# Kernel optimization log

Hardware: AMD Instinct MI355X
Metric: run time of the kernel (lower is better)

Reference implementation:

```python
import jax, jax.numpy as jnp
import numpy as np

SQRT_2_OVER_PI = 0.7978845608028654

def gelu_tanh(x):
    return 0.5 * x * (1.0 + jnp.tanh(SQRT_2_OVER_PI * (x + 0.044715 * x ** 3)))

def setup_inputs() -> dict:
    key = jax.random.key(0)
    ks = jax.random.split(key, 16)
    B, L, H, Dk, Dv = 4, 512, 8, 64, 64
    dm = H * Dk
    inp = {
        'q': jax.random.normal(ks[0], (B, L, dm), jnp.float32),
        'k': jax.random.normal(ks[1], (B, L, dm), jnp.float32),
        'v': jax.random.normal(ks[2], (B, L, dm), jnp.float32),
        'vec_adj_k': jax.random.normal(ks[3], (B, L, L, Dk), jnp.float32),
        'vec_adj_v': jax.random.normal(ks[4], (B, L, L, Dv), jnp.float32),
        'adj_k': jax.random.randint(ks[5], (B, L, L), 0, 2, jnp.int32),
        'adj_v': jax.random.randint(ks[6], (B, L, L), 0, 2, jnp.int32),
        # learned params (Linear weights stored as [in, out]; y = x @ W)
        'w_qs': jax.random.normal(ks[7], (dm, H * Dk), jnp.float32) * 0.02,
        'w_ks': jax.random.normal(ks[8], (dm, H * Dk), jnp.float32) * 0.02,
        'w_vs': jax.random.normal(ks[9], (dm, H * Dv), jnp.float32) * 0.02,
        'w_fc': jax.random.normal(ks[10], (H * Dk, H * Dk), jnp.float32) * 0.02,
        'w_nw': jax.random.normal(ks[11], (H * Dk, 1), jnp.float32) * 0.02,
        'w_self': jax.random.normal(ks[12], (H * Dk, H * Dk), jnp.float32) * 0.02,
        'w_dd': jax.random.normal(ks[13], (H * Dk, H * Dk), jnp.float32) * 0.02,
    }
    return inp

def reference(q, k, v, vec_adj_k, vec_adj_v, adj_k, adj_v,
              w_qs, w_ks, w_vs, w_fc, w_nw, w_self, w_dd):
    H, Dk, Dv = 8, 64, 64
    B, L, dm = q.shape
    temperature = Dk ** 0.5
    residual = q
    # projections -> [B, H, L, D]
    qh = (q @ w_qs).reshape(B, L, H, Dk).transpose(0, 2, 1, 3)
    kh = (k @ w_ks).reshape(B, L, H, Dk).transpose(0, 2, 1, 3)
    vh = (v @ w_vs).reshape(B, L, H, Dv).transpose(0, 2, 1, 3)
    qs = qh / temperature
    # inner_(q, k, vec_adj_k, flag=True): content + relative-position scores
    scores = jnp.einsum('bhld,bhmd->bhlm', qs, kh) \
           + jnp.einsum('bhld,blmd->bhlm', qs, vec_adj_k)  # [B,H,L,L]
    # adjacency mask (mask == 0 -> -10000)
    scores = jnp.where(adj_k[:, None, :, :] == 0, jnp.float32(-10000.0), scores)
    attn = jax.nn.softmax(scores, axis=-1)
    # inner_(attn, v, vec_adj_v, flag=False)
    out = jnp.einsum('bhlm,bhmd->bhld', attn, vh) \
        + jnp.einsum('bhlm,blmd->bhld', attn, vec_adj_v)
    qc = out.transpose(0, 2, 1, 3).reshape(B, L, H * Dv)  # [B,L,dm]
    # masked neighbor aggregation (GNN stage)
    adj_f = adj_k.astype(qc.dtype)
    nn_num = adj_f.sum(-1)                                  # [B,L]
    denom = jnp.where(nn_num >= 1.0, nn_num, 1.0)
    node_weight = jax.nn.sigmoid((qc @ w_nw)[..., 0])       # [B,L]
    self_info = qc @ w_self
    dd_info = qc @ w_dd
    dd_weight = node_weight[:, None, :] * adj_f             # [B,L,L]
    agg = jnp.matmul(dd_weight, dd_info) / denom[..., None]
    qo = gelu_tanh((self_info + agg) @ w_fc)
    qo = residual + qo
    return (qo, attn)
```

## Files before the change

kernel.cpp:

```cpp
#include <hip/hip_runtime.h>
#include <cstdint>

#define NB 4
#define NL 512
#define NH 8
#define ND 64
#define NDM 512

typedef __attribute__((ext_vector_type(8))) short short8;
typedef __attribute__((ext_vector_type(4))) float f32x4;

__device__ __forceinline__ unsigned short f2bf(float f){
  union { float f; unsigned u; } v; v.f = f;
  unsigned r = (v.u + 0x7fffu + ((v.u >> 16) & 1u)) >> 16;
  return (unsigned short)r;
}

__device__ __forceinline__ short8 ld8(const unsigned short* p){
  return *(const short8*)p;
}

__device__ __forceinline__ f32x4 mfma16(short8 a, short8 b, f32x4 c){
  return __builtin_amdgcn_mfma_f32_16x16x32_bf16(a, b, c, 0, 0, 0);
}

__device__ __forceinline__ float gelu_tanh(float x){
  float u = 0.7978845608028654f * (x + 0.044715f * x * x * x);
  return 0.5f * x * (1.f + tanhf(u));
}

__global__ __launch_bounds__(256) void k_cvt_in(const float* __restrict__ q,
    const float* __restrict__ k, const float* __restrict__ v,
    unsigned short* __restrict__ dst){
  int i = blockIdx.x * 256 + threadIdx.x;
  int w = i >> 18, r = i & 262143;
  const float* src = (w == 0) ? q : (w == 1) ? k : v;
  float4 f = *(const float4*)(src + (size_t)r * 4);
  unsigned lo = (unsigned)f2bf(f.x) | ((unsigned)f2bf(f.y) << 16);
  unsigned hi = (unsigned)f2bf(f.z) | ((unsigned)f2bf(f.w) << 16);
  uint2 o; o.x = lo; o.y = hi;
  *(uint2*)(dst + (size_t)w * 1048576 + (size_t)r * 4) = o;
}

__global__ __launch_bounds__(256) void k_cvt_w(const float* __restrict__ wqs,
    const float* __restrict__ wks, const float* __restrict__ wvs,
    const float* __restrict__ wself, const float* __restrict__ wdd,
    const float* __restrict__ wfc, unsigned short* __restrict__ Wt){
  int i = blockIdx.x * 256 + threadIdx.x;
  int w = i >> 18, r = i & 262143;
  const float* src = (w == 0) ? wqs : (w == 1) ? wks : (w == 2) ? wvs :
                     (w == 3) ? wself : (w == 4) ? wdd : wfc;
  int kk = r >> 9, n = r & 511;
  Wt[(size_t)w * 262144 + (size_t)n * 512 + kk] = f2bf(src[r]);
}

__global__ __launch_bounds__(256) void k_proj(const unsigned short* __restrict__ X,
    const unsigned short* __restrict__ W, unsigned short* __restrict__ dst, int mode){
  int wid = blockIdx.x * 4 + (threadIdx.x >> 6);
  int lane = threadIdx.x & 63;
  int tm = wid >> 5, tn = wid & 31;
  int r = lane & 15, q = lane >> 4;
  const unsigned short* A  = X + (size_t)(tm * 16 + r) * 512 + q * 8;
  const unsigned short* Bp = W + (size_t)(tn * 16 + r) * 512 + q * 8;
  f32x4 acc = {0.f, 0.f, 0.f, 0.f};
  for (int k = 0; k < 512; k += 32) acc = mfma16(ld8(A + k), ld8(Bp + k), acc);
  int col = tn * 16 + r;
  int h = col >> 6, d = col & 63;
  float sc = (mode == 0) ? 0.125f : 1.0f;
  for (int i = 0; i < 4; i++){
    int row = tm * 16 + q * 4 + i;
    int b = row >> 9, l = row & 511;
    float vv = acc[i] * sc;
    size_t idx = (mode == 2) ? ((size_t)((b * 8 + h) * 64 + d) * 512 + l)
                             : ((size_t)((b * 8 + h) * 512 + l) * 64 + d);
    dst[idx] = f2bf(vv);
  }
}

__global__ __launch_bounds__(256) void k_scores(const unsigned short* __restrict__ qs,
    const unsigned short* __restrict__ kh, float* __restrict__ attnF){
  int wid = blockIdx.x * 4 + (threadIdx.x >> 6);
  int lane = threadIdx.x & 63;
  int bh = wid >> 10, tile = wid & 1023;
  int tm = tile >> 5, tn = tile & 31;
  int r = lane & 15, q = lane >> 4;
  const unsigned short* A  = qs + (size_t)bh * 512 * 64 + (size_t)(tm * 16 + r) * 64 + q * 8;
  const unsigned short* Bp = kh + (size_t)bh * 512 * 64 + (size_t)(tn * 16 + r) * 64 + q * 8;
  f32x4 acc = {0.f, 0.f, 0.f, 0.f};
  acc = mfma16(ld8(A),      ld8(Bp),      acc);
  acc = mfma16(ld8(A + 32), ld8(Bp + 32), acc);
  float* C = attnF + (size_t)bh * 512 * 512;
  for (int i = 0; i < 4; i++){
    int row = tm * 16 + q * 4 + i;
    C[(size_t)row * 512 + tn * 16 + r] = acc[i];
  }
}

__global__ __launch_bounds__(256) void k_relsoft(const unsigned short* __restrict__ qs,
    const float* __restrict__ vak, const int* __restrict__ adj,
    float* __restrict__ attnF, unsigned short* __restrict__ attn_bf){
  int bid = blockIdx.x;
  int b = bid >> 9, l = bid & 511;
  int t = threadIdx.x, lane = t & 63, w = t >> 6;
  __shared__ __align__(16) unsigned short qsA[16 * 64];
  __shared__ __align__(16) unsigned short vkt[128 * 72];
  __shared__ float sc[8 * 512];
  __shared__ int adjs[512];
  for (int j = 0; j < 4; j++){
    int e = t + j * 256;
    int m = e >> 6, d = e & 63;
    qsA[e] = (m < 8) ? qs[((size_t)((b * 8 + m) * 512 + l)) * 64 + d] : (unsigned short)0;
  }
  for (int j = 0; j < 16; j++){
    int e = t + j * 256;
    int h = e >> 9, m = e & 511;
    sc[e] = attnF[((size_t)(b * 8 + h) * 512 + l) * 512 + m];
  }
  adjs[t]       = adj[(size_t)bid * 512 + t];
  adjs[t + 256] = adj[(size_t)bid * 512 + t + 256];
  __syncthreads();
  int r = lane & 15, q = lane >> 4;
  short8 a0 = ld8(qsA + r * 64 + q * 8);
  short8 a1 = ld8(qsA + r * 64 + 32 + q * 8);
  const float* vrow = vak + (size_t)bid * 512 * 64;
  for (int c = 0; c < 4; c++){
    for (int it = 0; it < 16; it++){
      int i2 = it * 256 + t;
      int m = i2 >> 5, d2 = (i2 & 31) * 2;
      const float2 f = *(const float2*)(vrow + (size_t)(c * 128 + m) * 64 + d2);
      unsigned pack = (unsigned)f2bf(f.x) | ((unsigned)f2bf(f.y) << 16);
      *(unsigned*)(&vkt[m * 72 + d2]) = pack;
    }
    __syncthreads();
    for (int nt2 = 0; nt2 < 2; nt2++){
      int nt = w * 2 + nt2;
      const unsigned short* bp = vkt + (nt * 16 + r) * 72 + q * 8;
      f32x4 acc = {0.f, 0.f, 0.f, 0.f};
      acc = mfma16(a0, ld8(bp),      acc);
      acc = mfma16(a1, ld8(bp + 32), acc);
      if (q < 2){
        for (int i = 0; i < 4; i++){
          int h = q * 4 + i;
          sc[h * 512 + c * 128 + nt * 16 + r] += acc[i];
        }
      }
    }
    __syncthreads();
  }
  for (int hh = 0; hh < 2; hh++){
    int h = w * 2 + hh;
    float v[8]; float mx = -3.0e38f;
    for (int i = 0; i < 8; i++){
      int m = lane + i * 64;
      float s = sc[h * 512 + m];
      if (adjs[m] == 0) s = -10000.0f;
      v[i] = s; mx = fmaxf(mx, s);
    }
    for (int off = 32; off; off >>= 1) mx = fmaxf(mx, __shfl_xor(mx, off, 64));
    float sum = 0.f;
    for (int i = 0; i < 8; i++){ v[i] = __expf(v[i] - mx); sum += v[i]; }
    for (int off = 32; off; off >>= 1) sum += __shfl_xor(sum, off, 64);
    float inv = 1.f / sum;
    size_t base = ((size_t)(b * 8 + h) * 512 + l) * 512;
    for (int i = 0; i < 8; i++){
      int m = lane + i * 64;
      float p2 = v[i] * inv;
      attnF[base + m] = p2;
      attn_bf[base + m] = f2bf(p2);
    }
  }
}

__global__ __launch_bounds__(256) void k_outc(const unsigned short* __restrict__ attn_bf,
    const unsigned short* __restrict__ vhT, float* __restrict__ qc){
  int wid = blockIdx.x * 4 + (threadIdx.x >> 6);
  int lane = threadIdx.x & 63;
  int bh = wid >> 7, tile = wid & 127;
  int tm = tile >> 2, tn = tile & 3;
  int r = lane & 15, q = lane >> 4;
  const unsigned short* A  = attn_bf + (size_t)bh * 512 * 512 + (size_t)(tm * 16 + r) * 512 + q * 8;
  const unsigned short* Bp = vhT + (size_t)bh * 64 * 512 + (size_t)(tn * 16 + r) * 512 + q * 8;
  f32x4 acc = {0.f, 0.f, 0.f, 0.f};
  for (int k = 0; k < 512; k += 32) acc = mfma16(ld8(A + k), ld8(Bp + k), acc);
  int b = bh >> 3, h = bh & 7;
  int d = tn * 16 + r;
  for (int i = 0; i < 4; i++){
    int lrow = tm * 16 + q * 4 + i;
    qc[(size_t)(b * 512 + lrow) * 512 + h * 64 + d] = acc[i];
  }
}

__global__ __launch_bounds__(256) void k_outrel(const unsigned short* __restrict__ attn_bf,
    const float* __restrict__ vav, const float* __restrict__ qc,
    const int* __restrict__ adj, const float* __restrict__ wnw,
    unsigned short* __restrict__ qc_bf, float* __restrict__ nw, float* __restrict__ invden){
  int bid = blockIdx.x;
  int b = bid >> 9, l = bid & 511;
  int t = threadIdx.x, lane = t & 63, w = t >> 6;
  __shared__ __align__(16) unsigned short vvT[64 * 136];
  __shared__ float orL[512];
  __shared__ float redf[4];
  __shared__ int redi[4];
  int r = lane & 15, q = lane >> 4;
  int h8 = r & 7;
  const float* vrow = vav + (size_t)bid * 512 * 64;
  const unsigned short* arow = attn_bf + ((size_t)(b * 8 + h8) * 512 + l) * 512;
  f32x4 acc = {0.f, 0.f, 0.f, 0.f};
  for (int c = 0; c < 4; c++){
    for (int it = 0; it < 16; it++){
      int i2 = it * 256 + t;
      int m = i2 >> 5, d2 = (i2 & 31) * 2;
      const float2 f = *(const float2*)(vrow + (size_t)(c * 128 + m) * 64 + d2);
      vvT[d2 * 136 + m]       = f2bf(f.x);
      vvT[(d2 + 1) * 136 + m] = f2bf(f.y);
    }
    __syncthreads();
    for (int s = 0; s < 4; s++){
      int kk = c * 128 + s * 32;
      short8 av = ld8(arow + kk + q * 8);
      short8 bv = ld8(vvT + (w * 16 + r) * 136 + s * 32 + q * 8);
      acc = mfma16(av, bv, acc);
    }
    __syncthreads();
  }
  if (q < 2){
    for (int i = 0; i < 4; i++){
      int h = q * 4 + i;
      orL[h * 64 + w * 16 + r] = acc[i];
    }
  }
  __syncthreads();
  float part = 0.f; int asum = 0;
  for (int j = 0; j < 2; j++){
    int e = t + j * 256;
    float val = qc[(size_t)bid * 512 + e] + orL[e];
    qc_bf[(size_t)bid * 512 + e] = f2bf(val);
    part += val * wnw[e];
    asum += adj[(size_t)bid * 512 + e];
  }
  for (int off = 32; off; off >>= 1){
    part += __shfl_xor(part, off, 64);
    asum += __shfl_xor(asum, off, 64);
  }
  if (lane == 0){ redf[w] = part; redi[w] = asum; }
  __syncthreads();
  if (t == 0){
    float tot = redf[0] + redf[1] + redf[2] + redf[3];
    int at = redi[0] + redi[1] + redi[2] + redi[3];
    nw[bid] = 1.f / (1.f + __expf(-tot));
    invden[bid] = 1.f / ((at >= 1) ? (float)at : 1.f);
  }
}

__global__ __launch_bounds__(256) void k_ddw(const int* __restrict__ adj,
    const float* __restrict__ nw, const float* __restrict__ invden,
    unsigned short* __restrict__ ddw){
  int i = blockIdx.x * 256 + threadIdx.x;
  int b = i >> 18, rest = i & 262143;
  int l = rest >> 9, m = rest & 511;
  int a = adj[i];
  float v = a ? nw[b * 512 + m] * invden[b * 512 + l] : 0.f;
  ddw[i] = f2bf(v);
}

__global__ __launch_bounds__(256) void k_gnn(const unsigned short* __restrict__ qcb,
    const unsigned short* __restrict__ W, float* __restrict__ outf,
    unsigned short* __restrict__ outT, int mode){
  int wid = blockIdx.x * 4 + (threadIdx.x >> 6);
  int lane = threadIdx.x & 63;
  int tm = wid >> 5, tn = wid & 31;
  int r = lane & 15, q = lane >> 4;
  const unsigned short* A  = qcb + (size_t)(tm * 16 + r) * 512 + q * 8;
  const unsigned short* Bp = W + (size_t)(tn * 16 + r) * 512 + q * 8;
  f32x4 acc = {0.f, 0.f, 0.f, 0.f};
  for (int k = 0; k < 512; k += 32) acc = mfma16(ld8(A + k), ld8(Bp + k), acc);
  int col = tn * 16 + r;
  for (int i = 0; i < 4; i++){
    int row = tm * 16 + q * 4 + i;
    if (mode == 0) outf[(size_t)row * 512 + col] = acc[i];
    else {
      int b = row >> 9, m = row & 511;
      outT[((size_t)(b * 512 + col)) * 512 + m] = f2bf(acc[i]);
    }
  }
}

__global__ __launch_bounds__(256) void k_agg(const unsigned short* __restrict__ ddw,
    const unsigned short* __restrict__ ddT, const float* __restrict__ selfi,
    unsigned short* __restrict__ xbf){
  int wid = blockIdx.x * 4 + (threadIdx.x >> 6);
  int lane = threadIdx.x & 63;
  int b = wid >> 10, tile = wid & 1023;
  int tm = tile >> 5, tn = tile & 31;
  int r = lane & 15, q = lane >> 4;
  const unsigned short* A  = ddw + (size_t)b * 262144 + (size_t)(tm * 16 + r) * 512 + q * 8;
  const unsigned short* Bp = ddT + (size_t)b * 262144 + (size_t)(tn * 16 + r) * 512 + q * 8;
  f32x4 acc = {0.f, 0.f, 0.f, 0.f};
  for (int k = 0; k < 512; k += 32) acc = mfma16(ld8(A + k), ld8(Bp + k), acc);
  int col = tn * 16 + r;
  for (int i = 0; i < 4; i++){
    int row = b * 512 + tm * 16 + q * 4 + i;
    float x = acc[i] + selfi[(size_t)row * 512 + col];
    xbf[(size_t)row * 512 + col] = f2bf(x);
  }
}

__global__ __launch_bounds__(256) void k_fc(const unsigned short* __restrict__ xbf,
    const unsigned short* __restrict__ W, const float* __restrict__ qin,
    float* __restrict__ qo){
  int wid = blockIdx.x * 4 + (threadIdx.x >> 6);
  int lane = threadIdx.x & 63;
  int tm = wid >> 5, tn = wid & 31;
  int r = lane & 15, q = lane >> 4;
  const unsigned short* A  = xbf + (size_t)(tm * 16 + r) * 512 + q * 8;
  const unsigned short* Bp = W + (size_t)(tn * 16 + r) * 512 + q * 8;
  f32x4 acc = {0.f, 0.f, 0.f, 0.f};
  for (int k = 0; k < 512; k += 32) acc = mfma16(ld8(A + k), ld8(Bp + k), acc);
  int col = tn * 16 + r;
  for (int i = 0; i < 4; i++){
    int row = tm * 16 + q * 4 + i;
    qo[(size_t)row * 512 + col] = qin[(size_t)row * 512 + col] + gelu_tanh(acc[i]);
  }
}

extern "C" void kernel_launch(void* const* d_in, const int* in_sizes, int n_in,
                              void* d_out, int out_size, void* d_ws, size_t ws_size,
                              hipStream_t stream){
  const float* q    = (const float*)d_in[0];
  const float* k    = (const float*)d_in[1];
  const float* v    = (const float*)d_in[2];
  const float* vak  = (const float*)d_in[3];
  const float* vav  = (const float*)d_in[4];
  const int*   adjk = (const int*)d_in[5];
  const float* wqs  = (const float*)d_in[7];
  const float* wks  = (const float*)d_in[8];
  const float* wvs  = (const float*)d_in[9];
  const float* wfc  = (const float*)d_in[10];
  const float* wnw  = (const float*)d_in[11];
  const float* wself= (const float*)d_in[12];
  const float* wdd  = (const float*)d_in[13];

  float* qo    = (float*)d_out;
  float* attnF = qo + 1048576;

  char* p = (char*)d_ws;
  unsigned short* xin   = (unsigned short*)p; p += 6291456;
  unsigned short* Wt    = (unsigned short*)p; p += 3145728;
  unsigned short* qsb   = (unsigned short*)p; p += 2097152;
  unsigned short* khb   = (unsigned short*)p; p += 2097152;
  unsigned short* vhT   = (unsigned short*)p; p += 2097152;
  unsigned short* attnb = (unsigned short*)p; p += 16777216;
  float*          qc    = (float*)p;          p += 4194304;
  unsigned short* qcb   = (unsigned short*)p; p += 2097152;
  float*          nw    = (float*)p;          p += 8192;
  float*          invd  = (float*)p;          p += 8192;
  float*          selfi = (float*)p;          p += 4194304;
  unsigned short* ddT   = (unsigned short*)p; p += 2097152;
  unsigned short* ddw   = (unsigned short*)p; p += 2097152;
  unsigned short* xbf   = (unsigned short*)p; p += 2097152;

  k_cvt_in<<<3072, 256, 0, stream>>>(q, k, v, xin);
  k_cvt_w<<<6144, 256, 0, stream>>>(wqs, wks, wvs, wself, wdd, wfc, Wt);
  k_proj<<<1024, 256, 0, stream>>>(xin,           Wt,          qsb, 0);
  k_proj<<<1024, 256, 0, stream>>>(xin + 1048576, Wt + 262144, khb, 1);
  k_proj<<<1024, 256, 0, stream>>>(xin + 2097152, Wt + 524288, vhT, 2);
  k_scores<<<8192, 256, 0, stream>>>(qsb, khb, attnF);
  k_relsoft<<<2048, 256, 0, stream>>>(qsb, vak, adjk, attnF, attnb);
  k_outc<<<1024, 256, 0, stream>>>(attnb, vhT, qc);
  k_outrel<<<2048, 256, 0, stream>>>(attnb, vav, qc, adjk, wnw, qcb, nw, invd);
  k_ddw<<<4096, 256, 0, stream>>>(adjk, nw, invd, ddw);
  k_gnn<<<1024, 256, 0, stream>>>(qcb, Wt + 786432,  selfi, (unsigned short*)nullptr, 0);
  k_gnn<<<1024, 256, 0, stream>>>(qcb, Wt + 1048576, (float*)nullptr, ddT, 1);
  k_agg<<<1024, 256, 0, stream>>>(ddw, ddT, selfi, xbf);
  k_fc<<<1024, 256, 0, stream>>>(xbf, Wt + 1310720, q, qo);
}
```

Before: 742.3 us.

## Fuse attention-value relative term into softmax kernel and merge launches

Moves the attn·vec_adj_v product into the softmax kernel, where the attention row is still in shared memory, so a separate pass no longer re-reads the bf16 attention. The vec_adj_k conversion now happens in registers and skips the LDS staging. Weight transposes go through a shared-memory tile for coalescing, and the input/weight conversions, the three projections and the two GNN GEMMs each become one launch. The ddw matrix is now built on the fly inside the aggregation GEMM. The new vec_adj_v loads are strided scalar reads, and the aggregation kernel recomputes the adjacency weights for every output column tile.

```diff
diff --git a/kernel.cpp b/kernel.cpp
--- a/kernel.cpp
+++ b/kernel.cpp
@@ -1,79 +1,87 @@
 #include <hip/hip_runtime.h>
 #include <cstdint>
 
-#define NB 4
-#define NL 512
-#define NH 8
-#define ND 64
-#define NDM 512
-
 typedef __attribute__((ext_vector_type(8))) short short8;
 typedef __attribute__((ext_vector_type(4))) float f32x4;
 
 __device__ __forceinline__ unsigned short f2bf(float f){
   union { float f; unsigned u; } v; v.f = f;
-  unsigned r = (v.u + 0x7fffu + ((v.u >> 16) & 1u)) >> 16;
-  return (unsigned short)r;
-}
-
-__device__ __forceinline__ short8 ld8(const unsigned short* p){
-  return *(const short8*)p;
-}
-
+  return (unsigned short)((v.u + 0x7fffu + ((v.u >> 16) & 1u)) >> 16);
+}
+__device__ __forceinline__ short8 ld8(const unsigned short* p){ return *(const short8*)p; }
 __device__ __forceinline__ f32x4 mfma16(short8 a, short8 b, f32x4 c){
   return __builtin_amdgcn_mfma_f32_16x16x32_bf16(a, b, c, 0, 0, 0);
 }
-
+__device__ __forceinline__ short8 cvt8(float4 a, float4 b){
+  short8 r;
+  r[0]=f2bf(a.x); r[1]=f2bf(a.y); r[2]=f2bf(a.z); r[3]=f2bf(a.w);
+  r[4]=f2bf(b.x); r[5]=f2bf(b.y); r[6]=f2bf(b.z); r[7]=f2bf(b.w);
+  return r;
+}
 __device__ __forceinline__ float gelu_tanh(float x){
   float u = 0.7978845608028654f * (x + 0.044715f * x * x * x);
   return 0.5f * x * (1.f + tanhf(u));
 }
 
-__global__ __launch_bounds__(256) void k_cvt_in(const float* __restrict__ q,
+__global__ __launch_bounds__(256) void k_prep(const float* __restrict__ q,
     const float* __restrict__ k, const float* __restrict__ v,
-    unsigned short* __restrict__ dst){
-  int i = blockIdx.x * 256 + threadIdx.x;
-  int w = i >> 18, r = i & 262143;
-  const float* src = (w == 0) ? q : (w == 1) ? k : v;
-  float4 f = *(const float4*)(src + (size_t)r * 4);
-  unsigned lo = (unsigned)f2bf(f.x) | ((unsigned)f2bf(f.y) << 16);
-  unsigned hi = (unsigned)f2bf(f.z) | ((unsigned)f2bf(f.w) << 16);
-  uint2 o; o.x = lo; o.y = hi;
-  *(uint2*)(dst + (size_t)w * 1048576 + (size_t)r * 4) = o;
-}
-
-__global__ __launch_bounds__(256) void k_cvt_w(const float* __restrict__ wqs,
-    const float* __restrict__ wks, const float* __restrict__ wvs,
-    const float* __restrict__ wself, const float* __restrict__ wdd,
-    const float* __restrict__ wfc, unsigned short* __restrict__ Wt){
-  int i = blockIdx.x * 256 + threadIdx.x;
-  int w = i >> 18, r = i & 262143;
-  const float* src = (w == 0) ? wqs : (w == 1) ? wks : (w == 2) ? wvs :
-                     (w == 3) ? wself : (w == 4) ? wdd : wfc;
-  int kk = r >> 9, n = r & 511;
-  Wt[(size_t)w * 262144 + (size_t)n * 512 + kk] = f2bf(src[r]);
-}
-
-__global__ __launch_bounds__(256) void k_proj(const unsigned short* __restrict__ X,
-    const unsigned short* __restrict__ W, unsigned short* __restrict__ dst, int mode){
-  int wid = blockIdx.x * 4 + (threadIdx.x >> 6);
+    const float* __restrict__ w0, const float* __restrict__ w1,
+    const float* __restrict__ w2, const float* __restrict__ w3,
+    const float* __restrict__ w4, const float* __restrict__ w5,
+    unsigned short* __restrict__ xin, unsigned short* __restrict__ Wt){
+  __shared__ unsigned short tl[64 * 72];
+  int bid = blockIdx.x, t = threadIdx.x;
+  if (bid < 3072){
+    int i = bid * 256 + t;
+    int w = i >> 18, r = i & 262143;
+    const float* src = (w == 0) ? q : (w == 1) ? k : v;
+    float4 f = *(const float4*)(src + (size_t)r * 4);
+    unsigned lo = (unsigned)f2bf(f.x) | ((unsigned)f2bf(f.y) << 16);
+    unsigned hi = (unsigned)f2bf(f.z) | ((unsigned)f2bf(f.w) << 16);
+    uint2 o; o.x = lo; o.y = hi;
+    *(uint2*)(xin + (size_t)w * 1048576 + (size_t)r * 4) = o;
+  } else {
+    int b2 = bid - 3072;
+    int mat = b2 >> 6, tile = b2 & 63;
+    int kt = tile >> 3, nt = tile & 7;
+    const float* src = (mat == 0) ? w0 : (mat == 1) ? w1 : (mat == 2) ? w2 :
+                       (mat == 3) ? w3 : (mat == 4) ? w4 : w5;
+    int c = t & 63, r0 = t >> 6;
+    for (int j = 0; j < 16; j++){
+      int kl = r0 * 16 + j;
+      tl[c * 72 + kl] = f2bf(src[(size_t)(kt * 64 + kl) * 512 + nt * 64 + c]);
+    }
+    __syncthreads();
+    unsigned short* dst = Wt + (size_t)mat * 262144;
+    for (int j = 0; j < 16; j++){
+      int nl = r0 * 16 + j;
+      dst[(size_t)(nt * 64 + nl) * 512 + kt * 64 + c] = tl[nl * 72 + c];
+    }
+  }
+}
+
+__global__ __launch_bounds__(256) void k_proj(const unsigned short* __restrict__ xin,
+    const unsigned short* __restrict__ Wt, unsigned short* __restrict__ qsb,
+    unsigned short* __restrict__ khb, unsigned short* __restrict__ vhT){
+  int mode = blockIdx.x >> 10;
+  int wid = (blockIdx.x & 1023) * 4 + (threadIdx.x >> 6);
   int lane = threadIdx.x & 63;
   int tm = wid >> 5, tn = wid & 31;
   int r = lane & 15, q = lane >> 4;
-  const unsigned short* A  = X + (size_t)(tm * 16 + r) * 512 + q * 8;
-  const unsigned short* Bp = W + (size_t)(tn * 16 + r) * 512 + q * 8;
+  const unsigned short* A  = xin + (size_t)mode * 1048576 + (size_t)(tm * 16 + r) * 512 + q * 8;
+  const unsigned short* Bp = Wt  + (size_t)mode * 262144  + (size_t)(tn * 16 + r) * 512 + q * 8;
   f32x4 acc = {0.f, 0.f, 0.f, 0.f};
   for (int k = 0; k < 512; k += 32) acc = mfma16(ld8(A + k), ld8(Bp + k), acc);
   int col = tn * 16 + r;
   int h = col >> 6, d = col & 63;
   float sc = (mode == 0) ? 0.125f : 1.0f;
+  unsigned short* dst = (mode == 0) ? qsb : (mode == 1) ? khb : vhT;
   for (int i = 0; i < 4; i++){
     int row = tm * 16 + q * 4 + i;
     int b = row >> 9, l = row & 511;
-    float vv = acc[i] * sc;
     size_t idx = (mode == 2) ? ((size_t)((b * 8 + h) * 64 + d) * 512 + l)
                              : ((size_t)((b * 8 + h) * 512 + l) * 64 + d);
-    dst[idx] = f2bf(vv);
+    dst[idx] = f2bf(acc[i] * sc);
   }
 }
 
@@ -84,32 +92,33 @@
   int bh = wid >> 10, tile = wid & 1023;
   int tm = tile >> 5, tn = tile & 31;
   int r = lane & 15, q = lane >> 4;
-  const unsigned short* A  = qs + (size_t)bh * 512 * 64 + (size_t)(tm * 16 + r) * 64 + q * 8;
-  const unsigned short* Bp = kh + (size_t)bh * 512 * 64 + (size_t)(tn * 16 + r) * 64 + q * 8;
+  const unsigned short* A  = qs + (size_t)bh * 32768 + (size_t)(tm * 16 + r) * 64 + q * 8;
+  const unsigned short* Bp = kh + (size_t)bh * 32768 + (size_t)(tn * 16 + r) * 64 + q * 8;
   f32x4 acc = {0.f, 0.f, 0.f, 0.f};
   acc = mfma16(ld8(A),      ld8(Bp),      acc);
   acc = mfma16(ld8(A + 32), ld8(Bp + 32), acc);
-  float* C = attnF + (size_t)bh * 512 * 512;
-  for (int i = 0; i < 4; i++){
-    int row = tm * 16 + q * 4 + i;
-    C[(size_t)row * 512 + tn * 16 + r] = acc[i];
-  }
-}
-
-__global__ __launch_bounds__(256) void k_relsoft(const unsigned short* __restrict__ qs,
-    const float* __restrict__ vak, const int* __restrict__ adj,
-    float* __restrict__ attnF, unsigned short* __restrict__ attn_bf){
+  float* C = attnF + (size_t)bh * 262144;
+  for (int i = 0; i < 4; i++)
+    C[(size_t)(tm * 16 + q * 4 + i) * 512 + tn * 16 + r] = acc[i];
+}
+
+__global__ __launch_bounds__(256) void k_attn(const unsigned short* __restrict__ qsb,
+    const float* __restrict__ vak, const float* __restrict__ vav,
+    const int* __restrict__ adj, float* __restrict__ attnF,
+    unsigned short* __restrict__ attnb, float* __restrict__ orel){
   int bid = blockIdx.x;
   int b = bid >> 9, l = bid & 511;
   int t = threadIdx.x, lane = t & 63, w = t >> 6;
-  __shared__ __align__(16) unsigned short qsA[16 * 64];
-  __shared__ __align__(16) unsigned short vkt[128 * 72];
+  int r = lane & 15, q = lane >> 4;
+  __shared__ __align__(16) unsigned short qsA[16 * 72];
   __shared__ float sc[8 * 512];
   __shared__ int adjs[512];
-  for (int j = 0; j < 4; j++){
-    int e = t + j * 256;
-    int m = e >> 6, d = e & 63;
-    qsA[e] = (m < 8) ? qs[((size_t)((b * 8 + m) * 512 + l)) * 64 + d] : (unsigned short)0;
+  __shared__ __align__(16) unsigned short pb[16 * 520];
+  for (int i = 0; i < 4; i++){
+    int m = w * 4 + i;
+    unsigned short vle = 0;
+    if (m < 8) vle = qsb[((size_t)((b * 8 + m) * 512 + l)) * 64 + lane];
+    qsA[m * 72 + lane] = vle;
   }
   for (int j = 0; j < 16; j++){
     int e = t + j * 256;
@@ -119,56 +128,61 @@
   adjs[t]       = adj[(size_t)bid * 512 + t];
   adjs[t + 256] = adj[(size_t)bid * 512 + t + 256];
   __syncthreads();
-  int r = lane & 15, q = lane >> 4;
-  short8 a0 = ld8(qsA + r * 64 + q * 8);
-  short8 a1 = ld8(qsA + r * 64 + 32 + q * 8);
-  const float* vrow = vak + (size_t)bid * 512 * 64;
-  for (int c = 0; c < 4; c++){
-    for (int it = 0; it < 16; it++){
-      int i2 = it * 256 + t;
-      int m = i2 >> 5, d2 = (i2 & 31) * 2;
-      const float2 f = *(const float2*)(vrow + (size_t)(c * 128 + m) * 64 + d2);
-      unsigned pack = (unsigned)f2bf(f.x) | ((unsigned)f2bf(f.y) << 16);
-      *(unsigned*)(&vkt[m * 72 + d2]) = pack;
-    }
-    __syncthreads();
-    for (int nt2 = 0; nt2 < 2; nt2++){
-      int nt = w * 2 + nt2;
-      const unsigned short* bp = vkt + (nt * 16 + r) * 72 + q * 8;
-      f32x4 acc = {0.f, 0.f, 0.f, 0.f};
-      acc = mfma16(a0, ld8(bp),      acc);
-      acc = mfma16(a1, ld8(bp + 32), acc);
-      if (q < 2){
-        for (int i = 0; i < 4; i++){
-          int h = q * 4 + i;
-          sc[h * 512 + c * 128 + nt * 16 + r] += acc[i];
-        }
-      }
-    }
-    __syncthreads();
-  }
+  short8 a0 = ld8(qsA + r * 72 + q * 8);
+  short8 a1 = ld8(qsA + r * 72 + 32 + q * 8);
+  const float* vrow = vak + (size_t)bid * 32768;
+  for (int tt = 0; tt < 8; tt++){
+    int nt = w * 8 + tt;
+    const float* bp = vrow + (size_t)(nt * 16 + r) * 64 + q * 8;
+    float4 f0 = *(const float4*)(bp);
+    float4 f1 = *(const float4*)(bp + 4);
+    float4 f2 = *(const float4*)(bp + 32);
+    float4 f3 = *(const float4*)(bp + 36);
+    f32x4 acc = {0.f, 0.f, 0.f, 0.f};
+    acc = mfma16(a0, cvt8(f0, f1), acc);
+    acc = mfma16(a1, cvt8(f2, f3), acc);
+    if (q < 2)
+      for (int i = 0; i < 4; i++) sc[(q * 4 + i) * 512 + nt * 16 + r] += acc[i];
+  }
+  __syncthreads();
   for (int hh = 0; hh < 2; hh++){
     int h = w * 2 + hh;
-    float v[8]; float mx = -3.0e38f;
+    float vv[8]; float mx = -3.0e38f;
     for (int i = 0; i < 8; i++){
       int m = lane + i * 64;
       float s = sc[h * 512 + m];
       if (adjs[m] == 0) s = -10000.0f;
-      v[i] = s; mx = fmaxf(mx, s);
+      vv[i] = s; mx = fmaxf(mx, s);
     }
     for (int off = 32; off; off >>= 1) mx = fmaxf(mx, __shfl_xor(mx, off, 64));
     float sum = 0.f;
-    for (int i = 0; i < 8; i++){ v[i] = __expf(v[i] - mx); sum += v[i]; }
+    for (int i = 0; i < 8; i++){ vv[i] = __expf(vv[i] - mx); sum += vv[i]; }
     for (int off = 32; off; off >>= 1) sum += __shfl_xor(sum, off, 64);
     float inv = 1.f / sum;
     size_t base = ((size_t)(b * 8 + h) * 512 + l) * 512;
     for (int i = 0; i < 8; i++){
       int m = lane + i * 64;
-      float p2 = v[i] * inv;
-      attnF[base + m] = p2;
-      attn_bf[base + m] = f2bf(p2);
-    }
-  }
+      float p = vv[i] * inv;
+      attnF[base + m] = p;
+      unsigned short pbf = f2bf(p);
+      attnb[base + m] = pbf;
+      pb[h * 520 + m] = pbf;
+    }
+  }
+  __syncthreads();
+  const float* vvrow = vav + (size_t)bid * 32768;
+  int dcol = w * 16 + r;
+  f32x4 acc = {0.f, 0.f, 0.f, 0.f};
+  for (int kb = 0; kb < 16; kb++){
+    int m0 = kb * 32 + q * 8;
+    short8 bf;
+    for (int j = 0; j < 8; j++) bf[j] = f2bf(vvrow[(size_t)(m0 + j) * 64 + dcol]);
+    short8 af = ld8(pb + r * 520 + kb * 32 + q * 8);
+    acc = mfma16(af, bf, acc);
+  }
+  if (q < 2)
+    for (int i = 0; i < 4; i++)
+      orel[(size_t)bid * 512 + (q * 4 + i) * 64 + dcol] = acc[i];
 }
 
 __global__ __launch_bounds__(256) void k_outc(const unsigned short* __restrict__ attn_bf,
@@ -178,8 +192,8 @@
   int bh = wid >> 7, tile = wid & 127;
   int tm = tile >> 2, tn = tile & 3;
   int r = lane & 15, q = lane >> 4;
-  const unsigned short* A  = attn_bf + (size_t)bh * 512 * 512 + (size_t)(tm * 16 + r) * 512 + q * 8;
-  const unsigned short* Bp = vhT + (size_t)bh * 64 * 512 + (size_t)(tn * 16 + r) * 512 + q * 8;
+  const unsigned short* A  = attn_bf + (size_t)bh * 262144 + (size_t)(tm * 16 + r) * 512 + q * 8;
+  const unsigned short* Bp = vhT + (size_t)bh * 32768 + (size_t)(tn * 16 + r) * 512 + q * 8;
   f32x4 acc = {0.f, 0.f, 0.f, 0.f};
   for (int k = 0; k < 512; k += 32) acc = mfma16(ld8(A + k), ld8(Bp + k), acc);
   int b = bh >> 3, h = bh & 7;
@@ -190,51 +204,18 @@
   }
 }
 
-__global__ __launch_bounds__(256) void k_outrel(const unsigned short* __restrict__ attn_bf,
-    const float* __restrict__ vav, const float* __restrict__ qc,
-    const int* __restrict__ adj, const float* __restrict__ wnw,
-    unsigned short* __restrict__ qc_bf, float* __restrict__ nw, float* __restrict__ invden){
-  int bid = blockIdx.x;
-  int b = bid >> 9, l = bid & 511;
-  int t = threadIdx.x, lane = t & 63, w = t >> 6;
-  __shared__ __align__(16) unsigned short vvT[64 * 136];
-  __shared__ float orL[512];
+__global__ __launch_bounds__(256) void k_fin(const float* __restrict__ qc,
+    const float* __restrict__ orel, const int* __restrict__ adj,
+    const float* __restrict__ wnw, unsigned short* __restrict__ qcb,
+    float* __restrict__ nw, float* __restrict__ invd){
+  int bid = blockIdx.x, t = threadIdx.x, lane = t & 63, w = t >> 6;
   __shared__ float redf[4];
   __shared__ int redi[4];
-  int r = lane & 15, q = lane >> 4;
-  int h8 = r & 7;
-  const float* vrow = vav + (size_t)bid * 512 * 64;
-  const unsigned short* arow = attn_bf + ((size_t)(b * 8 + h8) * 512 + l) * 512;
-  f32x4 acc = {0.f, 0.f, 0.f, 0.f};
-  for (int c = 0; c < 4; c++){
-    for (int it = 0; it < 16; it++){
-      int i2 = it * 256 + t;
-      int m = i2 >> 5, d2 = (i2 & 31) * 2;
-      const float2 f = *(const float2*)(vrow + (size_t)(c * 128 + m) * 64 + d2);
-      vvT[d2 * 136 + m]       = f2bf(f.x);
-      vvT[(d2 + 1) * 136 + m] = f2bf(f.y);
-    }
-    __syncthreads();
-    for (int s = 0; s < 4; s++){
-      int kk = c * 128 + s * 32;
-      short8 av = ld8(arow + kk + q * 8);
-      short8 bv = ld8(vvT + (w * 16 + r) * 136 + s * 32 + q * 8);
-      acc = mfma16(av, bv, acc);
-    }
-    __syncthreads();
-  }
-  if (q < 2){
-    for (int i = 0; i < 4; i++){
-      int h = q * 4 + i;
-      orL[h * 64 + w * 16 + r] = acc[i];
-    }
-  }
-  __syncthreads();
   float part = 0.f; int asum = 0;
   for (int j = 0; j < 2; j++){
     int e = t + j * 256;
-    float val = qc[(size_t)bid * 512 + e] + orL[e];
-    qc_bf[(size_t)bid * 512 + e] = f2bf(val);
+    float val = qc[(size_t)bid * 512 + e] + orel[(size_t)bid * 512 + e];
+    qcb[(size_t)bid * 512 + e] = f2bf(val);
     part += val * wnw[e];
     asum += adj[(size_t)bid * 512 + e];
   }
@@ -248,44 +229,35 @@
     float tot = redf[0] + redf[1] + redf[2] + redf[3];
     int at = redi[0] + redi[1] + redi[2] + redi[3];
     nw[bid] = 1.f / (1.f + __expf(-tot));
-    invden[bid] = 1.f / ((at >= 1) ? (float)at : 1.f);
-  }
-}
-
-__global__ __launch_bounds__(256) void k_ddw(const int* __restrict__ adj,
-    const float* __restrict__ nw, const float* __restrict__ invden,
-    unsigned short* __restrict__ ddw){
-  int i = blockIdx.x * 256 + threadIdx.x;
-  int b = i >> 18, rest = i & 262143;
-  int l = rest >> 9, m = rest & 511;
-  int a = adj[i];
-  float v = a ? nw[b * 512 + m] * invden[b * 512 + l] : 0.f;
-  ddw[i] = f2bf(v);
+    invd[bid] = 1.f / ((at >= 1) ? (float)at : 1.f);
+  }
 }
 
 __global__ __launch_bounds__(256) void k_gnn(const unsigned short* __restrict__ qcb,
-    const unsigned short* __restrict__ W, float* __restrict__ outf,
-    unsigned short* __restrict__ outT, int mode){
-  int wid = blockIdx.x * 4 + (threadIdx.x >> 6);
+    const unsigned short* __restrict__ Wt, float* __restrict__ selfi,
+    unsigned short* __restrict__ ddT){
+  int mode = blockIdx.x >> 10;
+  int wid = (blockIdx.x & 1023) * 4 + (threadIdx.x >> 6);
   int lane = threadIdx.x & 63;
   int tm = wid >> 5, tn = wid & 31;
   int r = lane & 15, q = lane >> 4;
   const unsigned short* A  = qcb + (size_t)(tm * 16 + r) * 512 + q * 8;
-  const unsigned short* Bp = W + (size_t)(tn * 16 + r) * 512 + q * 8;
+  const unsigned short* Bp = Wt + (size_t)(3 + mode) * 262144 + (size_t)(tn * 16 + r) * 512 + q * 8;
   f32x4 acc = {0.f, 0.f, 0.f, 0.f};
   for (int k = 0; k < 512; k += 32) acc = mfma16(ld8(A + k), ld8(Bp + k), acc);
   int col = tn * 16 + r;
   for (int i = 0; i < 4; i++){
     int row = tm * 16 + q * 4 + i;
-    if (mode == 0) outf[(size_t)row * 512 + col] = acc[i];
+    if (mode == 0) selfi[(size_t)row * 512 + col] = acc[i];
     else {
       int b = row >> 9, m = row & 511;
-      outT[((size_t)(b * 512 + col)) * 512 + m] = f2bf(acc[i]);
-    }
-  }
-}
-
-__global__ __launch_bounds__(256) void k_agg(const unsigned short* __restrict__ ddw,
+      ddT[((size_t)(b * 512 + col)) * 512 + m] = f2bf(acc[i]);
+    }
+  }
+}
+
+__global__ __launch_bounds__(256) void k_agg(const int* __restrict__ adj,
+    const float* __restrict__ nw, const float* __restrict__ invd,
     const unsigned short* __restrict__ ddT, const float* __restrict__ selfi,
     unsigned short* __restrict__ xbf){
   int wid = blockIdx.x * 4 + (threadIdx.x >> 6);
@@ -293,10 +265,21 @@
   int b = wid >> 10, tile = wid & 1023;
   int tm = tile >> 5, tn = tile & 31;
   int r = lane & 15, q = lane >> 4;
-  const unsigned short* A  = ddw + (size_t)b * 262144 + (size_t)(tm * 16 + r) * 512 + q * 8;
+  int lrow = tm * 16 + r;
+  float idv = invd[b * 512 + lrow];
+  const int* arow = adj + ((size_t)b * 512 + lrow) * 512;
+  const float* nwb = nw + b * 512;
   const unsigned short* Bp = ddT + (size_t)b * 262144 + (size_t)(tn * 16 + r) * 512 + q * 8;
   f32x4 acc = {0.f, 0.f, 0.f, 0.f};
-  for (int k = 0; k < 512; k += 32) acc = mfma16(ld8(A + k), ld8(Bp + k), acc);
+  for (int kk = 0; kk < 512; kk += 32){
+    int k0 = kk + q * 8;
+    short8 af;
+    for (int j = 0; j < 8; j++){
+      float vv = arow[k0 + j] ? nwb[k0 + j] * idv : 0.f;
+      af[j] = f2bf(vv);
+    }
+    acc = mfma16(af, ld8(Bp + kk), acc);
+  }
   int col = tn * 16 + r;
   for (int i = 0; i < 4; i++){
     int row = b * 512 + tm * 16 + q * 4 + i;
@@ -306,14 +289,14 @@
 }
 
 __global__ __launch_bounds__(256) void k_fc(const unsigned short* __restrict__ xbf,
-    const unsigned short* __restrict__ W, const float* __restrict__ qin,
+    const unsigned short* __restrict__ Wt, const float* __restrict__ qin,
     float* __restrict__ qo){
   int wid = blockIdx.x * 4 + (threadIdx.x >> 6);
   int lane = threadIdx.x & 63;
   int tm = wid >> 5, tn = wid & 31;
   int r = lane & 15, q = lane >> 4;
   const unsigned short* A  = xbf + (size_t)(tm * 16 + r) * 512 + q * 8;
-  const unsigned short* Bp = W + (size_t)(tn * 16 + r) * 512 + q * 8;
+  const unsigned short* Bp = Wt + (size_t)5 * 262144 + (size_t)(tn * 16 + r) * 512 + q * 8;
   f32x4 acc = {0.f, 0.f, 0.f, 0.f};
   for (int k = 0; k < 512; k += 32) acc = mfma16(ld8(A + k), ld8(Bp + k), acc);
   int col = tn * 16 + r;
@@ -351,26 +334,21 @@
   unsigned short* vhT   = (unsigned short*)p; p += 2097152;
   unsigned short* attnb = (unsigned short*)p; p += 16777216;
   float*          qc    = (float*)p;          p += 4194304;
+  float*          orel  = (float*)p;          p += 4194304;
   unsigned short* qcb   = (unsigned short*)p; p += 2097152;
   float*          nw    = (float*)p;          p += 8192;
   float*          invd  = (float*)p;          p += 8192;
   float*          selfi = (float*)p;          p += 4194304;
   unsigned short* ddT   = (unsigned short*)p; p += 2097152;
-  unsigned short* ddw   = (unsigned short*)p; p += 2097152;
   unsigned short* xbf   = (unsigned short*)p; p += 2097152;
 
-  k_cvt_in<<<3072, 256, 0, stream>>>(q, k, v, xin);
-  k_cvt_w<<<6144, 256, 0, stream>>>(wqs, wks, wvs, wself, wdd, wfc, Wt);
-  k_proj<<<1024, 256, 0, stream>>>(xin,           Wt,          qsb, 0);
-  k_proj<<<1024, 256, 0, stream>>>(xin + 1048576, Wt + 262144, khb, 1);
-  k_proj<<<1024, 256, 0, stream>>>(xin + 2097152, Wt + 524288, vhT, 2);
+  k_prep<<<3456, 256, 0, stream>>>(q, k, v, wqs, wks, wvs, wself, wdd, wfc, xin, Wt);
+  k_proj<<<3072, 256, 0, stream>>>(xin, Wt, qsb, khb, vhT);
   k_scores<<<8192, 256, 0, stream>>>(qsb, khb, attnF);
-  k_relsoft<<<2048, 256, 0, stream>>>(qsb, vak, adjk, attnF, attnb);
+  k_attn<<<2048, 256, 0, stream>>>(qsb, vak, vav, adjk, attnF, attnb, orel);
   k_outc<<<1024, 256, 0, stream>>>(attnb, vhT, qc);
-  k_outrel<<<2048, 256, 0, stream>>>(attnb, vav, qc, adjk, wnw, qcb, nw, invd);
-  k_ddw<<<4096, 256, 0, stream>>>(adjk, nw, invd, ddw);
-  k_gnn<<<1024, 256, 0, stream>>>(qcb, Wt + 786432,  selfi, (unsigned short*)nullptr, 0);
-  k_gnn<<<1024, 256, 0, stream>>>(qcb, Wt + 1048576, (float*)nullptr, ddT, 1);
-  k_agg<<<1024, 256, 0, stream>>>(ddw, ddT, selfi, xbf);
-  k_fc<<<1024, 256, 0, stream>>>(xbf, Wt + 1310720, q, qo);
-}
+  k_fin<<<2048, 256, 0, stream>>>(qc, orel, adjk, wnw, qcb, nw, invd);
+  k_gnn<<<2048, 256, 0, stream>>>(qcb, Wt, selfi, ddT);
+  k_agg<<<1024, 256, 0, stream>>>(adjk, nw, invd, ddT, selfi, xbf);
+  k_fc<<<1024, 256, 0, stream>>>(xbf, Wt, q, qo);
+}
```

Result: slower. 764.9 us (+3.0%).
